# Optimization experiments

Hardware: AMD Instinct MI355X
Metric: run time of the kernel (lower is better)

The kernel has to match this reference:

```python
import jax, jax.numpy as jnp
import numpy as np

N_RAYS = 8192
N_SAMPLES = 512  # hardcoded n_samples=512 in source
HID = 32
BOOSTER = 1.0


def setup_inputs() -> dict:
    key = jax.random.key(0)
    ks = jax.random.split(key, 8)
    # camera placed outside the box at z=-3, rays pointing toward +z into the aabb
    o = jnp.array([0.0, 0.0, -3.0]) + 0.05 * jax.random.normal(ks[0], (N_RAYS, 3))
    dxy = 0.5 * (2.0 * jax.random.uniform(ks[1], (N_RAYS, 2)) - 1.0)
    d = jnp.concatenate([dxy, jnp.ones((N_RAYS, 1))], axis=-1)  # unnormalized world dirs
    aabb = jnp.array([[-1.0, -1.0, -1.0], [1.0, 1.0, 1.0]])
    u = jax.random.uniform(ks[2], (N_RAYS, N_SAMPLES))  # stratified jitter
    W1 = 0.5 * jax.random.normal(ks[3], (3, HID))
    b1 = jnp.zeros((HID,))
    Wc = 0.2 * jax.random.normal(ks[4], (HID, 3))
    bc = jnp.zeros((3,))
    Wd = 0.2 * jax.random.normal(ks[5], (HID, 1))
    bd = jnp.zeros((1,))
    return dict(o=o, d=d, aabb=aabb, u=u, W1=W1, b1=b1, Wc=Wc, bc=bc, Wd=Wd, bd=bd)


def reference(o, d, aabb, u, W1, b1, Wc, bc, Wd, bd):
    # --- intersect_aabb (slab test) ---
    t1 = (aabb[0] - o) / d
    t2 = (aabb[1] - o) / d
    tnear = jnp.maximum(jnp.max(jnp.minimum(t1, t2), axis=-1), 0.0)  # [N]
    tfar = jnp.min(jnp.maximum(t1, t2), axis=-1)                      # [N]
    active = tnear < tfar                                             # [N] active_mask
    dnorm = jnp.linalg.norm(d, axis=-1, keepdims=True)                # [N,1]

    # --- sample_ray_step_stratified: T bins in [tnear, tfar], jittered ---
    idx = jnp.arange(N_SAMPLES, dtype=o.dtype)
    ts = tnear[:, None] + (tfar - tnear)[:, None] * (idx[None, :] + u) / N_SAMPLES  # [N,T]

    # --- query radiance field at xyz = o + d*ts ---
    xyz = o[:, None, :] + d[:, None, :] * ts[..., None]               # [N,T,3]
    ndc = 2.0 * (xyz - aabb[0]) / (aabb[1] - aabb[0]) - 1.0           # box-normalized
    inbox = jnp.all(jnp.abs(ndc) <= 1.0, axis=-1)                     # BoundsFilter.test
    h = jax.nn.relu(ndc @ W1 + b1)                                    # [N,T,HID]
    color = jax.nn.sigmoid(h @ Wc + bc)                               # [N,T,3]
    density = jax.nn.softplus(h @ Wd + bd)[..., 0]                    # [N,T]
    # masked scatter-back: out-of-box samples contribute zero
    density = jnp.where(inbox, density, 0.0)
    color = jnp.where(inbox[..., None], color, 0.0)

    # --- integrate_timesteps: alpha compositing with cumulative transmittance ---
    t_ext = jnp.concatenate([ts, (tfar + BOOSTER)[:, None]], axis=-1)
    delta = (t_ext[:, 1:] - t_ext[:, :-1]) * dnorm                    # [N,T]
    sd = density * delta
    trans = jnp.exp(-jnp.concatenate([jnp.zeros_like(sd[:, :1]), jnp.cumsum(sd[:, :-1], axis=-1)], axis=-1))
    w = trans * (1.0 - jnp.exp(-sd))                                  # weights [N,T]

    out_color = jnp.einsum('nt,ntc->nc', w, color)                    # color_map
    out_alpha = jnp.sum(w, axis=-1, keepdims=True)                    # alpha_map

    act = active[:, None].astype(o.dtype)                             # scatter to active rays only
    return jnp.concatenate([out_color * act, out_alpha * act], axis=-1)  # [N,4]
```

## Files before the change

### kernel.cpp

```cpp
#include <hip/hip_runtime.h>
#include <math.h>

#define NRAYS 8192
#define NS 512
#define HID 32
#define SPL 8

typedef float f32x2 __attribute__((ext_vector_type(2)));

__global__ __launch_bounds__(256) void render_kernel(
    const float* __restrict__ o_, const float* __restrict__ d_,
    const float* __restrict__ aabb, const float* __restrict__ u_,
    const float* __restrict__ W1, const float* __restrict__ b1,
    const float* __restrict__ Wc, const float* __restrict__ bc,
    const float* __restrict__ Wd, const float* __restrict__ bd,
    float* __restrict__ out)
{
    __shared__ float wsh[272];
    const int tid = threadIdx.x;

    if (tid < HID) {
        const int j = tid, p = j >> 1, h = j & 1;
        float* base = wsh + p * 16;
        base[0 + h]  = W1[0 * HID + j];
        base[2 + h]  = W1[1 * HID + j];
        base[4 + h]  = W1[2 * HID + j];
        base[6 + h]  = b1[j];
        base[8 + h]  = Wc[j * 3 + 0];
        base[10 + h] = Wc[j * 3 + 1];
        base[12 + h] = Wc[j * 3 + 2];
        base[14 + h] = Wd[j];
    } else if (tid == HID) {
        wsh[256] = bc[0]; wsh[257] = bc[1]; wsh[258] = bc[2]; wsh[259] = bd[0];
    }
    __syncthreads();

    const int lane = tid & 63;
    const int ray  = (blockIdx.x << 2) + (tid >> 6);
    if (ray >= NRAYS) return;

    const float ox = o_[ray * 3 + 0], oy = o_[ray * 3 + 1], oz = o_[ray * 3 + 2];
    const float dx = d_[ray * 3 + 0], dy = d_[ray * 3 + 1], dz = d_[ray * 3 + 2];
    const float lox = aabb[0], loy = aabb[1], loz = aabb[2];
    const float hix = aabb[3], hiy = aabb[4], hiz = aabb[5];

    float t1 = (lox - ox) / dx, t2 = (hix - ox) / dx;
    float tnear = fminf(t1, t2), tfar = fmaxf(t1, t2);
    t1 = (loy - oy) / dy; t2 = (hiy - oy) / dy;
    tnear = fmaxf(tnear, fminf(t1, t2)); tfar = fminf(tfar, fmaxf(t1, t2));
    t1 = (loz - oz) / dz; t2 = (hiz - oz) / dz;
    tnear = fmaxf(tnear, fminf(t1, t2)); tfar = fminf(tfar, fmaxf(t1, t2));
    tnear = fmaxf(tnear, 0.0f);

    float4 res = make_float4(0.0f, 0.0f, 0.0f, 0.0f);

    if (tnear < tfar) {
        const float dnorm = sqrtf(dx * dx + dy * dy + dz * dz);
        const float dt = (tfar - tnear) * (1.0f / (float)NS);
        const float sx = 2.0f / (hix - lox);
        const float sy = 2.0f / (hiy - loy);
        const float sz = 2.0f / (hiz - loz);
        const float bc0 = wsh[256], bc1 = wsh[257], bc2 = wsh[258], bd0 = wsh[259];

        const float cx = (ox - lox) * sx - 1.0f, gx = dx * sx;
        const float cy = (oy - loy) * sy - 1.0f, gy = dy * sy;
        const float cz = (oz - loz) * sz - 1.0f, gz = dz * sz;
        const f32x2 cx2 = {cx, cx}, cy2 = {cy, cy}, cz2 = {cz, cz};
        const f32x2 gx2 = {gx, gx}, gy2 = {gy, gy}, gz2 = {gz, gz};

        const int base_t = lane * SPL;
        const float* __restrict__ urow = u_ + (size_t)ray * NS + base_t;
        const float4 uaq = *reinterpret_cast<const float4*>(urow);
        const float4 ubq = *reinterpret_cast<const float4*>(urow + 4);
        float us[9];
        us[0] = uaq.x; us[1] = uaq.y; us[2] = uaq.z; us[3] = uaq.w;
        us[4] = ubq.x; us[5] = ubq.y; us[6] = ubq.z; us[7] = ubq.w;
        us[8] = __shfl_down(uaq.x, 1);

        float tsv[SPL], delta[SPL];
        #pragma unroll
        for (int s = 0; s < SPL; ++s) {
            const int t = base_t + s;
            tsv[s] = fmaf(dt, (float)t + us[s], tnear);
            float dl;
            if (t == NS - 1) dl = (tfar + 1.0f) - tsv[s];
            else             dl = dt * (1.0f + us[s + 1] - us[s]);
            delta[s] = dl * dnorm;
        }

        f32x2 cr2[SPL], cg2[SPL], cb2[SPL], dd2[SPL];
        #pragma unroll
        for (int s = 0; s < SPL; ++s) {
            cr2[s] = (f32x2){bc0, 0.0f};
            cg2[s] = (f32x2){bc1, 0.0f};
            cb2[s] = (f32x2){bc2, 0.0f};
            dd2[s] = (f32x2){bd0, 0.0f};
        }
        const float4* __restrict__ wq = reinterpret_cast<const float4*>(wsh);
        #pragma unroll 4
        for (int p = 0; p < HID / 2; ++p) {
            const float4 q0 = wq[p * 4 + 0];
            const float4 q1 = wq[p * 4 + 1];
            const float4 q2 = wq[p * 4 + 2];
            const float4 q3 = wq[p * 4 + 3];
            const f32x2 w1x = {q0.x, q0.y}, w1y = {q0.z, q0.w};
            const f32x2 w1z = {q1.x, q1.y}, b12 = {q1.z, q1.w};
            const f32x2 wcr = {q2.x, q2.y}, wcg = {q2.z, q2.w};
            const f32x2 wcb = {q3.x, q3.y}, wd2 = {q3.z, q3.w};
            const f32x2 A2 = __builtin_elementwise_fma(cx2, w1x,
                             __builtin_elementwise_fma(cy2, w1y,
                             __builtin_elementwise_fma(cz2, w1z, b12)));
            const f32x2 B2 = __builtin_elementwise_fma(gx2, w1x,
                             __builtin_elementwise_fma(gy2, w1y, gz2 * w1z));
            #pragma unroll
            for (int s = 0; s < SPL; ++s) {
                const f32x2 ts2 = {tsv[s], tsv[s]};
                f32x2 h2 = __builtin_elementwise_fma(ts2, B2, A2);
                h2 = __builtin_elementwise_max(h2, (f32x2){0.0f, 0.0f});
                cr2[s] = __builtin_elementwise_fma(h2, wcr, cr2[s]);
                cg2[s] = __builtin_elementwise_fma(h2, wcg, cg2[s]);
                cb2[s] = __builtin_elementwise_fma(h2, wcb, cb2[s]);
                dd2[s] = __builtin_elementwise_fma(h2, wd2, dd2[s]);
            }
        }

        float sd[SPL], csum[SPL];
        float cum = 0.0f;
        #pragma unroll
        for (int s = 0; s < SPL; ++s) {
            const float dd = dd2[s].x + dd2[s].y;
            const float dens = fmaxf(dd, 0.0f) + __logf(1.0f + __expf(-fabsf(dd)));
            sd[s] = dens * delta[s];
            cum += sd[s];
            csum[s] = cum;
        }

        float L = cum;
        #pragma unroll
        for (int off = 1; off < 64; off <<= 1) {
            const float v = __shfl_up(L, off);
            L += (lane >= off) ? v : 0.0f;
        }
        const float E = L - cum;

        float accR = 0.0f, accG = 0.0f, accB = 0.0f;
        const float e0 = __expf(-E);
        float eprev = e0;
        #pragma unroll
        for (int s = 0; s < SPL; ++s) {
            const float ecur = __expf(-(E + csum[s]));
            const float w = eprev - ecur;
            eprev = ecur;
            const float cr = cr2[s].x + cr2[s].y;
            const float cg = cg2[s].x + cg2[s].y;
            const float cb = cb2[s].x + cb2[s].y;
            const float colR = __builtin_amdgcn_rcpf(1.0f + __expf(-cr));
            const float colG = __builtin_amdgcn_rcpf(1.0f + __expf(-cg));
            const float colB = __builtin_amdgcn_rcpf(1.0f + __expf(-cb));
            accR = fmaf(w, colR, accR);
            accG = fmaf(w, colG, accG);
            accB = fmaf(w, colB, accB);
        }
        float accA = e0 - eprev;

        #pragma unroll
        for (int off = 32; off; off >>= 1) {
            accR += __shfl_xor(accR, off);
            accG += __shfl_xor(accG, off);
            accB += __shfl_xor(accB, off);
            accA += __shfl_xor(accA, off);
        }
        res = make_float4(accR, accG, accB, accA);
    }

    if (lane == 0) {
        reinterpret_cast<float4*>(out)[ray] = res;
    }
}

extern "C" void kernel_launch(void* const* d_in, const int* in_sizes, int n_in,
                              void* d_out, int out_size, void* d_ws, size_t ws_size,
                              hipStream_t stream) {
    const float* o_   = (const float*)d_in[0];
    const float* d_   = (const float*)d_in[1];
    const float* aabb = (const float*)d_in[2];
    const float* u_   = (const float*)d_in[3];
    const float* W1   = (const float*)d_in[4];
    const float* b1   = (const float*)d_in[5];
    const float* Wc   = (const float*)d_in[6];
    const float* bc   = (const float*)d_in[7];
    const float* Wd   = (const float*)d_in[8];
    const float* bd   = (const float*)d_in[9];
    float* out = (float*)d_out;

    render_kernel<<<NRAYS / 4, 256, 0, stream>>>(o_, d_, aabb, u_, W1, b1, Wc, bc, Wd, bd, out);
}
```

Before: 108.6 us.

## Split each ray across two waves with cross-wave transmittance handoff via LDS

Each ray is now handled by two wavefronts of four samples per lane instead of one wavefront of eight. The second wave takes the first wave's optical-depth total through shared memory, and the two partial color sums are combined in LDS. The MLP inner loop now packs pairs of samples into the f32x2 vector lanes instead of pairs of hidden units, which removes the final horizontal adds. The aim is more waves and parallelism with less register pressure, at the cost of redundant per-ray setup, two extra block barriers, and recomputing the first-layer A/B per hidden unit in scalar form.

```diff
diff --git a/kernel.cpp b/kernel.cpp
--- a/kernel.cpp
+++ b/kernel.cpp
@@ -4,7 +4,7 @@
 #define NRAYS 8192
 #define NS 512
 #define HID 32
-#define SPL 8
+#define SPL 4
 
 typedef float f32x2 __attribute__((ext_vector_type(2)));
 
@@ -16,28 +16,32 @@
     const float* __restrict__ Wd, const float* __restrict__ bd,
     float* __restrict__ out)
 {
-    __shared__ float wsh[272];
+    __shared__ float wsh[260];
+    __shared__ float wtot[2][2];
+    __shared__ float4 wpart[2][2];
     const int tid = threadIdx.x;
 
     if (tid < HID) {
-        const int j = tid, p = j >> 1, h = j & 1;
-        float* base = wsh + p * 16;
-        base[0 + h]  = W1[0 * HID + j];
-        base[2 + h]  = W1[1 * HID + j];
-        base[4 + h]  = W1[2 * HID + j];
-        base[6 + h]  = b1[j];
-        base[8 + h]  = Wc[j * 3 + 0];
-        base[10 + h] = Wc[j * 3 + 1];
-        base[12 + h] = Wc[j * 3 + 2];
-        base[14 + h] = Wd[j];
+        const int j = tid;
+        float* base = wsh + j * 8;
+        base[0] = W1[0 * HID + j];
+        base[1] = W1[1 * HID + j];
+        base[2] = W1[2 * HID + j];
+        base[3] = b1[j];
+        base[4] = Wc[j * 3 + 0];
+        base[5] = Wc[j * 3 + 1];
+        base[6] = Wc[j * 3 + 2];
+        base[7] = Wd[j];
     } else if (tid == HID) {
         wsh[256] = bc[0]; wsh[257] = bc[1]; wsh[258] = bc[2]; wsh[259] = bd[0];
     }
     __syncthreads();
 
     const int lane = tid & 63;
-    const int ray  = (blockIdx.x << 2) + (tid >> 6);
-    if (ray >= NRAYS) return;
+    const int wave = tid >> 6;
+    const int pair = wave >> 1;
+    const int half = wave & 1;
+    const int ray  = (blockIdx.x << 1) + pair;
 
     const float ox = o_[ray * 3 + 0], oy = o_[ray * 3 + 1], oz = o_[ray * 3 + 2];
     const float dx = d_[ray * 3 + 0], dy = d_[ray * 3 + 1], dz = d_[ray * 3 + 2];
@@ -52,9 +56,12 @@
     tnear = fmaxf(tnear, fminf(t1, t2)); tfar = fminf(tfar, fmaxf(t1, t2));
     tnear = fmaxf(tnear, 0.0f);
 
-    float4 res = make_float4(0.0f, 0.0f, 0.0f, 0.0f);
-
-    if (tnear < tfar) {
+    const bool active = (tnear < tfar);
+
+    float sd[SPL], csum[SPL], colR[SPL], colG[SPL], colB[SPL];
+    float Lsc = 0.0f, cum = 0.0f, T = 0.0f;
+
+    if (active) {
         const float dnorm = sqrtf(dx * dx + dy * dy + dz * dz);
         const float dt = (tfar - tnear) * (1.0f / (float)NS);
         const float sx = 2.0f / (hix - lox);
@@ -65,116 +72,119 @@
         const float cx = (ox - lox) * sx - 1.0f, gx = dx * sx;
         const float cy = (oy - loy) * sy - 1.0f, gy = dy * sy;
         const float cz = (oz - loz) * sz - 1.0f, gz = dz * sz;
-        const f32x2 cx2 = {cx, cx}, cy2 = {cy, cy}, cz2 = {cz, cz};
-        const f32x2 gx2 = {gx, gx}, gy2 = {gy, gy}, gz2 = {gz, gz};
-
-        const int base_t = lane * SPL;
-        const float* __restrict__ urow = u_ + (size_t)ray * NS + base_t;
-        const float4 uaq = *reinterpret_cast<const float4*>(urow);
-        const float4 ubq = *reinterpret_cast<const float4*>(urow + 4);
-        float us[9];
-        us[0] = uaq.x; us[1] = uaq.y; us[2] = uaq.z; us[3] = uaq.w;
-        us[4] = ubq.x; us[5] = ubq.y; us[6] = ubq.z; us[7] = ubq.w;
-        us[8] = __shfl_down(uaq.x, 1);
+
+        const int t0 = (half << 8) + (lane << 2);
+        const float* __restrict__ urow = u_ + (size_t)ray * NS;
+        const float4 ua = *reinterpret_cast<const float4*>(urow + t0);
+        const float unext = (t0 + 4 < NS) ? urow[t0 + 4] : 0.0f;
+        float us[5] = {ua.x, ua.y, ua.z, ua.w, unext};
 
         float tsv[SPL], delta[SPL];
         #pragma unroll
         for (int s = 0; s < SPL; ++s) {
-            const int t = base_t + s;
+            const int t = t0 + s;
             tsv[s] = fmaf(dt, (float)t + us[s], tnear);
-            float dl;
-            if (t == NS - 1) dl = (tfar + 1.0f) - tsv[s];
-            else             dl = dt * (1.0f + us[s + 1] - us[s]);
+            const float dl = (t == NS - 1) ? (tfar + 1.0f) - tsv[s]
+                                           : dt * (1.0f + us[s + 1] - us[s]);
             delta[s] = dl * dnorm;
         }
-
-        f32x2 cr2[SPL], cg2[SPL], cb2[SPL], dd2[SPL];
-        #pragma unroll
-        for (int s = 0; s < SPL; ++s) {
-            cr2[s] = (f32x2){bc0, 0.0f};
-            cg2[s] = (f32x2){bc1, 0.0f};
-            cb2[s] = (f32x2){bc2, 0.0f};
-            dd2[s] = (f32x2){bd0, 0.0f};
-        }
+        const f32x2 ts01 = {tsv[0], tsv[1]};
+        const f32x2 ts23 = {tsv[2], tsv[3]};
+
+        f32x2 cr01 = {bc0, bc0}, cr23 = {bc0, bc0};
+        f32x2 cg01 = {bc1, bc1}, cg23 = {bc1, bc1};
+        f32x2 cb01 = {bc2, bc2}, cb23 = {bc2, bc2};
+        f32x2 dd01 = {bd0, bd0}, dd23 = {bd0, bd0};
+
         const float4* __restrict__ wq = reinterpret_cast<const float4*>(wsh);
         #pragma unroll 4
-        for (int p = 0; p < HID / 2; ++p) {
-            const float4 q0 = wq[p * 4 + 0];
-            const float4 q1 = wq[p * 4 + 1];
-            const float4 q2 = wq[p * 4 + 2];
-            const float4 q3 = wq[p * 4 + 3];
-            const f32x2 w1x = {q0.x, q0.y}, w1y = {q0.z, q0.w};
-            const f32x2 w1z = {q1.x, q1.y}, b12 = {q1.z, q1.w};
-            const f32x2 wcr = {q2.x, q2.y}, wcg = {q2.z, q2.w};
-            const f32x2 wcb = {q3.x, q3.y}, wd2 = {q3.z, q3.w};
-            const f32x2 A2 = __builtin_elementwise_fma(cx2, w1x,
-                             __builtin_elementwise_fma(cy2, w1y,
-                             __builtin_elementwise_fma(cz2, w1z, b12)));
-            const f32x2 B2 = __builtin_elementwise_fma(gx2, w1x,
-                             __builtin_elementwise_fma(gy2, w1y, gz2 * w1z));
-            #pragma unroll
-            for (int s = 0; s < SPL; ++s) {
-                const f32x2 ts2 = {tsv[s], tsv[s]};
-                f32x2 h2 = __builtin_elementwise_fma(ts2, B2, A2);
-                h2 = __builtin_elementwise_max(h2, (f32x2){0.0f, 0.0f});
-                cr2[s] = __builtin_elementwise_fma(h2, wcr, cr2[s]);
-                cg2[s] = __builtin_elementwise_fma(h2, wcg, cg2[s]);
-                cb2[s] = __builtin_elementwise_fma(h2, wcb, cb2[s]);
-                dd2[s] = __builtin_elementwise_fma(h2, wd2, dd2[s]);
-            }
-        }
-
-        float sd[SPL], csum[SPL];
-        float cum = 0.0f;
+        for (int j = 0; j < HID; ++j) {
+            const float4 qa = wq[j * 2 + 0];
+            const float4 qb = wq[j * 2 + 1];
+            const float A = fmaf(cx, qa.x, fmaf(cy, qa.y, fmaf(cz, qa.z, qa.w)));
+            const float B = fmaf(gx, qa.x, fmaf(gy, qa.y, gz * qa.z));
+            const f32x2 A2 = {A, A}, B2 = {B, B};
+            f32x2 h01 = __builtin_elementwise_max(
+                __builtin_elementwise_fma(ts01, B2, A2), (f32x2){0.0f, 0.0f});
+            f32x2 h23 = __builtin_elementwise_max(
+                __builtin_elementwise_fma(ts23, B2, A2), (f32x2){0.0f, 0.0f});
+            const f32x2 wr = {qb.x, qb.x}, wg = {qb.y, qb.y};
+            const f32x2 wb = {qb.z, qb.z}, wd2 = {qb.w, qb.w};
+            cr01 = __builtin_elementwise_fma(h01, wr, cr01);
+            cr23 = __builtin_elementwise_fma(h23, wr, cr23);
+            cg01 = __builtin_elementwise_fma(h01, wg, cg01);
+            cg23 = __builtin_elementwise_fma(h23, wg, cg23);
+            cb01 = __builtin_elementwise_fma(h01, wb, cb01);
+            cb23 = __builtin_elementwise_fma(h23, wb, cb23);
+            dd01 = __builtin_elementwise_fma(h01, wd2, dd01);
+            dd23 = __builtin_elementwise_fma(h23, wd2, dd23);
+        }
+
+        const float ddv[SPL] = {dd01.x, dd01.y, dd23.x, dd23.y};
+        const float crv[SPL] = {cr01.x, cr01.y, cr23.x, cr23.y};
+        const float cgv[SPL] = {cg01.x, cg01.y, cg23.x, cg23.y};
+        const float cbv[SPL] = {cb01.x, cb01.y, cb23.x, cb23.y};
+
+        cum = 0.0f;
         #pragma unroll
         for (int s = 0; s < SPL; ++s) {
-            const float dd = dd2[s].x + dd2[s].y;
+            const float dd = ddv[s];
             const float dens = fmaxf(dd, 0.0f) + __logf(1.0f + __expf(-fabsf(dd)));
             sd[s] = dens * delta[s];
             cum += sd[s];
             csum[s] = cum;
-        }
-
-        float L = cum;
+            colR[s] = __builtin_amdgcn_rcpf(1.0f + __expf(-crv[s]));
+            colG[s] = __builtin_amdgcn_rcpf(1.0f + __expf(-cgv[s]));
+            colB[s] = __builtin_amdgcn_rcpf(1.0f + __expf(-cbv[s]));
+        }
+
+        Lsc = cum;
         #pragma unroll
         for (int off = 1; off < 64; off <<= 1) {
-            const float v = __shfl_up(L, off);
-            L += (lane >= off) ? v : 0.0f;
-        }
-        const float E = L - cum;
-
-        float accR = 0.0f, accG = 0.0f, accB = 0.0f;
+            const float v = __shfl_up(Lsc, off);
+            Lsc += (lane >= off) ? v : 0.0f;
+        }
+        T = __shfl(Lsc, 63);
+    }
+
+    if (lane == 0) wtot[pair][half] = T;
+    __syncthreads();
+
+    float4 partial = make_float4(0.0f, 0.0f, 0.0f, 0.0f);
+    if (active) {
+        const float E = (half ? wtot[pair][0] : 0.0f) + (Lsc - cum);
         const float e0 = __expf(-E);
         float eprev = e0;
+        float aR = 0.0f, aG = 0.0f, aB = 0.0f;
         #pragma unroll
         for (int s = 0; s < SPL; ++s) {
             const float ecur = __expf(-(E + csum[s]));
             const float w = eprev - ecur;
             eprev = ecur;
-            const float cr = cr2[s].x + cr2[s].y;
-            const float cg = cg2[s].x + cg2[s].y;
-            const float cb = cb2[s].x + cb2[s].y;
-            const float colR = __builtin_amdgcn_rcpf(1.0f + __expf(-cr));
-            const float colG = __builtin_amdgcn_rcpf(1.0f + __expf(-cg));
-            const float colB = __builtin_amdgcn_rcpf(1.0f + __expf(-cb));
-            accR = fmaf(w, colR, accR);
-            accG = fmaf(w, colG, accG);
-            accB = fmaf(w, colB, accB);
-        }
-        float accA = e0 - eprev;
+            aR = fmaf(w, colR[s], aR);
+            aG = fmaf(w, colG[s], aG);
+            aB = fmaf(w, colB[s], aB);
+        }
+        float aA = e0 - eprev;
 
         #pragma unroll
         for (int off = 32; off; off >>= 1) {
-            accR += __shfl_xor(accR, off);
-            accG += __shfl_xor(accG, off);
-            accB += __shfl_xor(accB, off);
-            accA += __shfl_xor(accA, off);
-        }
-        res = make_float4(accR, accG, accB, accA);
-    }
-
-    if (lane == 0) {
-        reinterpret_cast<float4*>(out)[ray] = res;
+            aR += __shfl_xor(aR, off);
+            aG += __shfl_xor(aG, off);
+            aB += __shfl_xor(aB, off);
+            aA += __shfl_xor(aA, off);
+        }
+        partial = make_float4(aR, aG, aB, aA);
+    }
+
+    if (lane == 0) wpart[pair][half] = partial;
+    __syncthreads();
+
+    if (half == 0 && lane == 0) {
+        const float4 p0 = wpart[pair][0];
+        const float4 p1 = wpart[pair][1];
+        reinterpret_cast<float4*>(out)[ray] =
+            make_float4(p0.x + p1.x, p0.y + p1.y, p0.z + p1.z, p0.w + p1.w);
     }
 }
 
@@ -193,5 +203,5 @@
     const float* bd   = (const float*)d_in[9];
     float* out = (float*)d_out;
 
-    render_kernel<<<NRAYS / 4, 256, 0, stream>>>(o_, d_, aabb, u_, W1, b1, Wc, bc, Wd, bd, out);
+    render_kernel<<<NRAYS / 2, 256, 0, stream>>>(o_, d_, aabb, u_, W1, b1, Wc, bc, Wd, bd, out);
 }
```

After: 111.2 us. 2.4% more time.

## Replace per-sample MLP with piecewise-linear breakpoint tables along each ray

Applied to the files above, without the earlier changes.

Along a ray, each hidden unit's pre-activation is linear in t, so the ReLU network's output is piecewise linear in t, with breakpoints where units switch on or off. Each wave computes the 32 breakpoints, sorts them with a bitonic network, prefix-sums the slope and intercept changes, and stores coefficient tables in shared memory. Each sample then evaluates one linear function after a binary and linear search, instead of a 32-wide hidden-layer dot product. This removes most per-sample FMAs but adds sorting, shuffles, shared memory traffic, a block barrier and possible divergence in the search loop. It may also change floating-point rounding.

```diff
diff --git a/kernel.cpp b/kernel.cpp
--- a/kernel.cpp
+++ b/kernel.cpp
@@ -16,28 +16,25 @@
     const float* __restrict__ Wd, const float* __restrict__ bd,
     float* __restrict__ out)
 {
-    __shared__ float wsh[272];
-    const int tid = threadIdx.x;
-
-    if (tid < HID) {
-        const int j = tid, p = j >> 1, h = j & 1;
-        float* base = wsh + p * 16;
-        base[0 + h]  = W1[0 * HID + j];
-        base[2 + h]  = W1[1 * HID + j];
-        base[4 + h]  = W1[2 * HID + j];
-        base[6 + h]  = b1[j];
-        base[8 + h]  = Wc[j * 3 + 0];
-        base[10 + h] = Wc[j * 3 + 1];
-        base[12 + h] = Wc[j * 3 + 2];
-        base[14 + h] = Wd[j];
-    } else if (tid == HID) {
-        wsh[256] = bc[0]; wsh[257] = bc[1]; wsh[258] = bc[2]; wsh[259] = bd[0];
-    }
-    __syncthreads();
-
+    __shared__ float  keyA[4][68];
+    __shared__ float4 cPA[4][33];
+    __shared__ float4 cQA[4][33];
+
+    const int tid  = threadIdx.x;
     const int lane = tid & 63;
-    const int ray  = (blockIdx.x << 2) + (tid >> 6);
-    if (ray >= NRAYS) return;
+    const int wv   = tid >> 6;
+    const int id   = lane & 31;
+    const int ray  = (blockIdx.x << 2) + wv;
+
+    const float w1x = W1[0 * HID + id];
+    const float w1y = W1[1 * HID + id];
+    const float w1z = W1[2 * HID + id];
+    const float b1j = b1[id];
+    const float wr  = Wc[id * 3 + 0];
+    const float wg  = Wc[id * 3 + 1];
+    const float wb  = Wc[id * 3 + 2];
+    const float wd  = Wd[id];
+    const float bc0 = bc[0], bc1 = bc[1], bc2 = bc[2], bd0 = bd[0];
 
     const float ox = o_[ray * 3 + 0], oy = o_[ray * 3 + 1], oz = o_[ray * 3 + 2];
     const float dx = d_[ray * 3 + 0], dy = d_[ray * 3 + 1], dz = d_[ray * 3 + 2];
@@ -52,21 +49,100 @@
     tnear = fmaxf(tnear, fminf(t1, t2)); tfar = fminf(tfar, fmaxf(t1, t2));
     tnear = fmaxf(tnear, 0.0f);
 
-    float4 res = make_float4(0.0f, 0.0f, 0.0f, 0.0f);
-
-    if (tnear < tfar) {
-        const float dnorm = sqrtf(dx * dx + dy * dy + dz * dz);
-        const float dt = (tfar - tnear) * (1.0f / (float)NS);
+    const bool active = (tnear < tfar);
+
+    if (active) {
         const float sx = 2.0f / (hix - lox);
         const float sy = 2.0f / (hiy - loy);
         const float sz = 2.0f / (hiz - loz);
-        const float bc0 = wsh[256], bc1 = wsh[257], bc2 = wsh[258], bd0 = wsh[259];
-
         const float cx = (ox - lox) * sx - 1.0f, gx = dx * sx;
         const float cy = (oy - loy) * sy - 1.0f, gy = dy * sy;
         const float cz = (oz - loz) * sz - 1.0f, gz = dz * sz;
-        const f32x2 cx2 = {cx, cx}, cy2 = {cy, cy}, cz2 = {cz, cz};
-        const f32x2 gx2 = {gx, gx}, gy2 = {gy, gy}, gz2 = {gz, gz};
+
+        const float A = fmaf(cx, w1x, fmaf(cy, w1y, fmaf(cz, w1z, b1j)));
+        const float B = fmaf(gx, w1x, fmaf(gy, w1y, gz * w1z));
+
+        float dP[4], dQ[4];
+        dP[0] = A * wr; dP[1] = A * wg; dP[2] = A * wb; dP[3] = A * wd;
+        dQ[0] = B * wr; dQ[1] = B * wg; dQ[2] = B * wb; dQ[3] = B * wd;
+
+        const bool act0 = fmaf(B, tnear, A) > 0.0f;
+        float base[8];
+        #pragma unroll
+        for (int c = 0; c < 4; ++c) {
+            base[c]     = act0 ? dP[c] : 0.0f;
+            base[c + 4] = act0 ? dQ[c] : 0.0f;
+        }
+        #pragma unroll
+        for (int m = 1; m <= 16; m <<= 1) {
+            #pragma unroll
+            for (int c = 0; c < 8; ++c) base[c] += __shfl_xor(base[c], m);
+        }
+
+        const float tb = -A / B;
+        const bool ev = (tb > tnear) && (tb < tfar) && (fabsf(tb) < 1e30f);
+        const float sgn = (B > 0.0f) ? 1.0f : -1.0f;
+        float key = ev ? tb : 3e38f;
+        float e[8];
+        #pragma unroll
+        for (int c = 0; c < 4; ++c) {
+            e[c]     = ev ? sgn * dP[c] : 0.0f;
+            e[c + 4] = ev ? sgn * dQ[c] : 0.0f;
+        }
+        int src = lane;
+
+        #pragma unroll
+        for (int k = 2; k <= 32; k <<= 1) {
+            #pragma unroll
+            for (int j = k >> 1; j >= 1; j >>= 1) {
+                const float pkey = __shfl_xor(key, j);
+                const int   psrc = __shfl_xor(src, j);
+                const bool up    = ((id & k) == 0);
+                const bool lower = ((id & j) == 0);
+                const bool pless = (pkey < key) || ((pkey == key) && (psrc < src));
+                const bool wantMin = (lower == up);
+                const bool take = wantMin ? pless : !pless;
+                key = take ? pkey : key;
+                src = take ? psrc : src;
+            }
+        }
+
+        float se[8];
+        #pragma unroll
+        for (int c = 0; c < 8; ++c)
+            se[c] = __int_as_float(__builtin_amdgcn_ds_bpermute(src << 2, __float_as_int(e[c])));
+
+        #pragma unroll
+        for (int off = 1; off < 32; off <<= 1) {
+            #pragma unroll
+            for (int c = 0; c < 8; ++c) {
+                const float v = __shfl_up(se[c], off);
+                se[c] += (id >= off) ? v : 0.0f;
+            }
+        }
+
+        if (lane < 32) {
+            keyA[wv][id + 1] = key;
+            cPA[wv][id + 1] = make_float4(base[0] + se[0], base[1] + se[1],
+                                          base[2] + se[2], base[3] + se[3]);
+            cQA[wv][id + 1] = make_float4(base[4] + se[4], base[5] + se[5],
+                                          base[6] + se[6], base[7] + se[7]);
+        }
+        if (lane == 0) {
+            keyA[wv][0] = -3e38f;
+            cPA[wv][0] = make_float4(base[0], base[1], base[2], base[3]);
+            cQA[wv][0] = make_float4(base[4], base[5], base[6], base[7]);
+        }
+        if (lane < 35) keyA[wv][33 + lane] = 3e38f;
+    }
+
+    __syncthreads();
+
+    float4 res = make_float4(0.0f, 0.0f, 0.0f, 0.0f);
+
+    if (active) {
+        const float dnorm = sqrtf(dx * dx + dy * dy + dz * dz);
+        const float dt = (tfar - tnear) * (1.0f / (float)NS);
 
         const int base_t = lane * SPL;
         const float* __restrict__ urow = u_ + (size_t)ray * NS + base_t;
@@ -82,57 +158,43 @@
         for (int s = 0; s < SPL; ++s) {
             const int t = base_t + s;
             tsv[s] = fmaf(dt, (float)t + us[s], tnear);
-            float dl;
-            if (t == NS - 1) dl = (tfar + 1.0f) - tsv[s];
-            else             dl = dt * (1.0f + us[s + 1] - us[s]);
+            const float dl = (t == NS - 1) ? (tfar + 1.0f) - tsv[s]
+                                           : dt * (1.0f + us[s + 1] - us[s]);
             delta[s] = dl * dnorm;
         }
 
-        f32x2 cr2[SPL], cg2[SPL], cb2[SPL], dd2[SPL];
+        const float* keys = &keyA[wv][0];
+
+        int k = 0;
+        {
+            const float t0v = tsv[0];
+            if (keys[k + 32] <= t0v) k += 32;
+            if (keys[k + 16] <= t0v) k += 16;
+            if (keys[k + 8]  <= t0v) k += 8;
+            if (keys[k + 4]  <= t0v) k += 4;
+            if (keys[k + 2]  <= t0v) k += 2;
+            if (keys[k + 1]  <= t0v) k += 1;
+        }
+
+        float sd[SPL], csum[SPL], cR[SPL], cG[SPL], cB[SPL];
+        float cum = 0.0f;
         #pragma unroll
         for (int s = 0; s < SPL; ++s) {
-            cr2[s] = (f32x2){bc0, 0.0f};
-            cg2[s] = (f32x2){bc1, 0.0f};
-            cb2[s] = (f32x2){bc2, 0.0f};
-            dd2[s] = (f32x2){bd0, 0.0f};
-        }
-        const float4* __restrict__ wq = reinterpret_cast<const float4*>(wsh);
-        #pragma unroll 4
-        for (int p = 0; p < HID / 2; ++p) {
-            const float4 q0 = wq[p * 4 + 0];
-            const float4 q1 = wq[p * 4 + 1];
-            const float4 q2 = wq[p * 4 + 2];
-            const float4 q3 = wq[p * 4 + 3];
-            const f32x2 w1x = {q0.x, q0.y}, w1y = {q0.z, q0.w};
-            const f32x2 w1z = {q1.x, q1.y}, b12 = {q1.z, q1.w};
-            const f32x2 wcr = {q2.x, q2.y}, wcg = {q2.z, q2.w};
-            const f32x2 wcb = {q3.x, q3.y}, wd2 = {q3.z, q3.w};
-            const f32x2 A2 = __builtin_elementwise_fma(cx2, w1x,
-                             __builtin_elementwise_fma(cy2, w1y,
-                             __builtin_elementwise_fma(cz2, w1z, b12)));
-            const f32x2 B2 = __builtin_elementwise_fma(gx2, w1x,
-                             __builtin_elementwise_fma(gy2, w1y, gz2 * w1z));
-            #pragma unroll
-            for (int s = 0; s < SPL; ++s) {
-                const f32x2 ts2 = {tsv[s], tsv[s]};
-                f32x2 h2 = __builtin_elementwise_fma(ts2, B2, A2);
-                h2 = __builtin_elementwise_max(h2, (f32x2){0.0f, 0.0f});
-                cr2[s] = __builtin_elementwise_fma(h2, wcr, cr2[s]);
-                cg2[s] = __builtin_elementwise_fma(h2, wcg, cg2[s]);
-                cb2[s] = __builtin_elementwise_fma(h2, wcb, cb2[s]);
-                dd2[s] = __builtin_elementwise_fma(h2, wd2, dd2[s]);
-            }
-        }
-
-        float sd[SPL], csum[SPL];
-        float cum = 0.0f;
-        #pragma unroll
-        for (int s = 0; s < SPL; ++s) {
-            const float dd = dd2[s].x + dd2[s].y;
-            const float dens = fmaxf(dd, 0.0f) + __logf(1.0f + __expf(-fabsf(dd)));
+            const float t = tsv[s];
+            while (keys[k + 1] <= t) ++k;
+            const float4 P = cPA[wv][k];
+            const float4 Q = cQA[wv][k];
+            const float crv = fmaf(Q.x, t, P.x) + bc0;
+            const float cgv = fmaf(Q.y, t, P.y) + bc1;
+            const float cbv = fmaf(Q.z, t, P.z) + bc2;
+            const float ddv = fmaf(Q.w, t, P.w) + bd0;
+            const float dens = fmaxf(ddv, 0.0f) + __logf(1.0f + __expf(-fabsf(ddv)));
             sd[s] = dens * delta[s];
             cum += sd[s];
             csum[s] = cum;
+            cR[s] = __builtin_amdgcn_rcpf(1.0f + __expf(-crv));
+            cG[s] = __builtin_amdgcn_rcpf(1.0f + __expf(-cgv));
+            cB[s] = __builtin_amdgcn_rcpf(1.0f + __expf(-cbv));
         }
 
         float L = cum;
@@ -143,7 +205,7 @@
         }
         const float E = L - cum;
 
-        float accR = 0.0f, accG = 0.0f, accB = 0.0f;
+        float aR = 0.0f, aG = 0.0f, aB = 0.0f;
         const float e0 = __expf(-E);
         float eprev = e0;
         #pragma unroll
@@ -151,26 +213,20 @@
             const float ecur = __expf(-(E + csum[s]));
             const float w = eprev - ecur;
             eprev = ecur;
-            const float cr = cr2[s].x + cr2[s].y;
-            const float cg = cg2[s].x + cg2[s].y;
-            const float cb = cb2[s].x + cb2[s].y;
-            const float colR = __builtin_amdgcn_rcpf(1.0f + __expf(-cr));
-            const float colG = __builtin_amdgcn_rcpf(1.0f + __expf(-cg));
-            const float colB = __builtin_amdgcn_rcpf(1.0f + __expf(-cb));
-            accR = fmaf(w, colR, accR);
-            accG = fmaf(w, colG, accG);
-            accB = fmaf(w, colB, accB);
-        }
-        float accA = e0 - eprev;
+            aR = fmaf(w, cR[s], aR);
+            aG = fmaf(w, cG[s], aG);
+            aB = fmaf(w, cB[s], aB);
+        }
+        float aA = e0 - eprev;
 
         #pragma unroll
         for (int off = 32; off; off >>= 1) {
-            accR += __shfl_xor(accR, off);
-            accG += __shfl_xor(accG, off);
-            accB += __shfl_xor(accB, off);
-            accA += __shfl_xor(accA, off);
-        }
-        res = make_float4(accR, accG, accB, accA);
+            aR += __shfl_xor(aR, off);
+            aG += __shfl_xor(aG, off);
+            aB += __shfl_xor(aB, off);
+            aA += __shfl_xor(aA, off);
+        }
+        res = make_float4(aR, aG, aB, aA);
     }
 
     if (lane == 0) {
```

New measurement: 99.83 us. 1.09x faster.
